# Performance work log

Hardware: AMD Instinct MI355X
Metric: run time of the kernel (lower is better)

The kernel has to match this reference:

```python
import jax, jax.numpy as jnp
import numpy as np

TEMPERATURE = 8.0  # sqrt(d_k=64)

def setup_inputs() -> dict:
    key = jax.random.key(0)
    kq, kk, kv = jax.random.split(key, 3)
    B, S, D = 32, 2048, 64  # B = batch*heads
    q = jax.random.normal(kq, (B, S, D), dtype=jnp.float32)
    k = jax.random.normal(kk, (B, S, D), dtype=jnp.float32)
    v = jax.random.normal(kv, (B, S, D), dtype=jnp.float32)
    return {"q": q, "k": k, "v": v}

def reference(q, k, v):
    # attn = softmax((q @ k^T) / temperature) along key dim; dropout = identity (eval)
    attn = jnp.einsum('bqd,bkd->bqk', q, k) / TEMPERATURE  # [B, S, S]
    attn = jax.nn.softmax(attn, axis=2)
    out = jnp.einsum('bqk,bkd->bqd', attn, v)              # [B, S, D]
    return out
```

## Files before the change

kernel.cpp:

```cpp
#include <hip/hip_runtime.h>
#include <stdint.h>


#define BATCH 32
#define SEQ   2048
#define DIM   64
#define QBLK_WAVE 32
#define NWAVES 4
#define QBLK  (QBLK_WAVE*NWAVES)
#define KVBLK 64
#define NT    (SEQ/KVBLK)
#define BUFSHORTS (KVBLK*DIM)

typedef __attribute__((ext_vector_type(8)))  __bf16   bf16x8;
typedef __attribute__((ext_vector_type(16))) float    f32x16;
typedef __attribute__((ext_vector_type(2)))  unsigned uint2v;
typedef __attribute__((ext_vector_type(4)))  unsigned uint4v;

static __device__ __forceinline__ unsigned cvt_pk(float lo, float hi) {
    unsigned r; asm("v_cvt_pk_bf16_f32 %0, %1, %2" : "=v"(r) : "v"(lo), "v"(hi)); return r;
}
static __device__ __forceinline__ float exp2v(float x) {
    float r; asm("v_exp_f32 %0, %1" : "=v"(r) : "v"(x)); return r;
}
static __device__ __forceinline__ float other_half(float v, int hi) {
    unsigned u = __builtin_bit_cast(unsigned, v);
    uint2v r = __builtin_amdgcn_permlane32_swap(u, u, false, false);
    return __builtin_bit_cast(float, hi ? r[0] : r[1]);
}

#define MFMA32(A, B, C) __builtin_amdgcn_mfma_f32_32x32x16_bf16((A), (B), (C), 0, 0, 0)
#define TRR(dst, OFFSTR) \
    asm volatile("ds_read_b64_tr_b16 %0, %1 offset:" OFFSTR : "=v"(dst) : "v"(trb))
#define MAX4(a,b,c,d) fmaxf(fmaxf((a),(b)), fmaxf((c),(d)))
#define SUM4(a,b,c,d) (((a)+(b)) + ((c)+(d)))

static __device__ __forceinline__ bf16x8 frag_of(uint2v r0, uint2v r1) {
    uint4v w = { r0[0], r0[1], r1[0], r1[1] };
    return __builtin_bit_cast(bf16x8, w);
}

__global__ __launch_bounds__(256, 2)
void attn_fwd_kernel(const float* __restrict__ q,
                     const float* __restrict__ k,
                     const float* __restrict__ v,
                     float* __restrict__ out)
{
    __shared__ unsigned short Ksh[2][BUFSHORTS];
    __shared__ unsigned short Vsh[2][BUFSHORTS];

    const int id    = blockIdx.x;
    const int swz   = (id & 7) * ((SEQ / QBLK) * BATCH / 8) + (id >> 3);
    const int batch = swz >> 4;
    const int qtile = swz & 15;

    const int t    = threadIdx.x;
    const int lane = t & 63;
    const int wid  = t >> 6;
    const int hi   = lane >> 5;
    const int l31  = lane & 31;
    const int l7   = lane & 7;

    const size_t bbase = (size_t)batch * SEQ * DIM;
    const int q0w = qtile * QBLK + wid * QBLK_WAVE;

    bf16x8 qf[4];
    {
        const float sc = 0.125f * 1.44269504088896341f;
        const float* qp = q + bbase + (size_t)(q0w + l31) * DIM + hi * 8;
        #pragma unroll
        for (int dblk = 0; dblk < 4; ++dblk) {
            float4 f0 = *(const float4*)(qp + dblk * 16);
            float4 f1 = *(const float4*)(qp + dblk * 16 + 4);
            uint4v w = { cvt_pk(f0.x * sc, f0.y * sc), cvt_pk(f0.z * sc, f0.w * sc),
                         cvt_pk(f1.x * sc, f1.y * sc), cvt_pk(f1.z * sc, f1.w * sc) };
            qf[dblk] = __builtin_bit_cast(bf16x8, w);
        }
    }

    const int srow = t >> 2, sq = t & 3;
    const float* kg = k + bbase + (size_t)srow * DIM + sq * 16;
    const float* vg = v + bbase + (size_t)srow * DIM + sq * 16;
    const int ch0 = ((2 * sq)     ^ (srow & 7)) * 8;
    const int ch1 = ((2 * sq + 1) ^ (srow & 7)) * 8;

    const int bq = (l31 & 15) >> 2, ee = (lane >> 4) & 1, cc = lane & 3;
    const unsigned vb = (unsigned)(uintptr_t)&Vsh[0][0];
    const unsigned trbase = vb + (unsigned)((8 * hi + bq) * 128 +
                                            (((2 * ee + (cc >> 1)) ^ bq) * 16) + (cc & 1) * 8);

    f32x16 oacc0, oacc1;
    #pragma unroll
    for (int r = 0; r < 16; ++r) { oacc0[r] = 0.f; oacc1[r] = 0.f; }
    float m_run = 0.0f, l_run = 0.0f;

    float4 rk[4], rv[4];
    #pragma unroll
    for (int i = 0; i < 4; ++i) {
        rk[i] = *(const float4*)(kg + i * 4);
        rv[i] = *(const float4*)(vg + i * 4);
    }
    {
        uint4v kw0 = { cvt_pk(rk[0].x, rk[0].y), cvt_pk(rk[0].z, rk[0].w),
                       cvt_pk(rk[1].x, rk[1].y), cvt_pk(rk[1].z, rk[1].w) };
        uint4v kw1 = { cvt_pk(rk[2].x, rk[2].y), cvt_pk(rk[2].z, rk[2].w),
                       cvt_pk(rk[3].x, rk[3].y), cvt_pk(rk[3].z, rk[3].w) };
        uint4v vw0 = { cvt_pk(rv[0].x, rv[0].y), cvt_pk(rv[0].z, rv[0].w),
                       cvt_pk(rv[1].x, rv[1].y), cvt_pk(rv[1].z, rv[1].w) };
        uint4v vw1 = { cvt_pk(rv[2].x, rv[2].y), cvt_pk(rv[2].z, rv[2].w),
                       cvt_pk(rv[3].x, rv[3].y), cvt_pk(rv[3].z, rv[3].w) };
        *(uint4v*)&Ksh[0][srow * DIM + ch0] = kw0;
        *(uint4v*)&Ksh[0][srow * DIM + ch1] = kw1;
        *(uint4v*)&Vsh[0][srow * DIM + ch0] = vw0;
        *(uint4v*)&Vsh[0][srow * DIM + ch1] = vw1;
    }
    #pragma unroll
    for (int i = 0; i < 4; ++i) {
        rk[i] = *(const float4*)(kg + KVBLK * DIM + i * 4);
        rv[i] = *(const float4*)(vg + KVBLK * DIM + i * 4);
    }
    asm volatile("s_waitcnt lgkmcnt(0)" ::: "memory");

    #pragma unroll 2
    for (int tile = 0; tile < NT; ++tile) {
        const int cur = tile & 1;
        __builtin_amdgcn_s_barrier();
        __builtin_amdgcn_sched_barrier(0);

        const unsigned short* krow = &Ksh[cur][l31 * DIM];
        const unsigned trb = trbase + (unsigned)(cur * (2 * BUFSHORTS));

        f32x16 s0, s1;
        #pragma unroll
        for (int r = 0; r < 16; ++r) { s0[r] = 0.f; s1[r] = 0.f; }
        __builtin_amdgcn_s_setprio(1);
        #pragma unroll
        for (int dblk = 0; dblk < 4; ++dblk) {
            int cofs = (((2 * dblk + hi) ^ l7) * 8);
            bf16x8 kf0 = *(const bf16x8*)&krow[cofs];
            bf16x8 kf1 = *(const bf16x8*)&krow[32 * DIM + cofs];
            s0 = MFMA32(kf0, qf[dblk], s0);
            s1 = MFMA32(kf1, qf[dblk], s1);
        }
        __builtin_amdgcn_s_setprio(0);

        uint2v m0k0r0, m0k0r1, m0k1r0, m0k1r1, m0k2r0, m0k2r1, m0k3r0, m0k3r1;
        uint2v m1k0r0, m1k0r1, m1k1r0, m1k1r1, m1k2r0, m1k2r1, m1k3r0, m1k3r1;
        TRR(m0k0r0, "0");    TRR(m0k0r1, "576");
        TRR(m0k1r0, "2048"); TRR(m0k1r1, "2624");
        TRR(m0k2r0, "4096"); TRR(m0k2r1, "4672");
        TRR(m0k3r0, "6144"); TRR(m0k3r1, "6720");
        TRR(m1k0r0, "64");   TRR(m1k0r1, "512");
        TRR(m1k1r0, "2112"); TRR(m1k1r1, "2560");
        TRR(m1k2r0, "4160"); TRR(m1k2r1, "4608");
        TRR(m1k3r0, "6208"); TRR(m1k3r1, "6656");

        {
            float a0 = MAX4(s0[0], s0[1], s0[2],  s0[3]);
            float a1 = MAX4(s0[4], s0[5], s0[6],  s0[7]);
            float a2 = MAX4(s0[8], s0[9], s0[10], s0[11]);
            float a3 = MAX4(s0[12], s0[13], s0[14], s0[15]);
            float b0 = MAX4(s1[0], s1[1], s1[2],  s1[3]);
            float b1 = MAX4(s1[4], s1[5], s1[6],  s1[7]);
            float b2 = MAX4(s1[8], s1[9], s1[10], s1[11]);
            float b3 = MAX4(s1[12], s1[13], s1[14], s1[15]);
            float pmax = MAX4(MAX4(a0, a1, a2, a3), b0, b1, b2);
            pmax = fmaxf(pmax, b3);
            pmax = fmaxf(pmax, other_half(pmax, hi));
            if (!__all(pmax - m_run <= 12.0f)) {
                float mn    = fmaxf(m_run, pmax);
                float alpha = exp2v(m_run - mn);
                m_run = mn;
                l_run *= alpha;
                #pragma unroll
                for (int r = 0; r < 16; ++r) { oacc0[r] *= alpha; oacc1[r] *= alpha; }
            }
        }
        #pragma unroll
        for (int r = 0; r < 16; ++r) s0[r] = exp2v(s0[r] - m_run);
        #pragma unroll
        for (int r = 0; r < 16; ++r) s1[r] = exp2v(s1[r] - m_run);
        {
            float a0 = SUM4(s0[0], s0[1], s0[2],  s0[3]);
            float a1 = SUM4(s0[4], s0[5], s0[6],  s0[7]);
            float a2 = SUM4(s0[8], s0[9], s0[10], s0[11]);
            float a3 = SUM4(s0[12], s0[13], s0[14], s0[15]);
            float b0 = SUM4(s1[0], s1[1], s1[2],  s1[3]);
            float b1 = SUM4(s1[4], s1[5], s1[6],  s1[7]);
            float b2 = SUM4(s1[8], s1[9], s1[10], s1[11]);
            float b3 = SUM4(s1[12], s1[13], s1[14], s1[15]);
            float rs = SUM4(SUM4(a0, a1, a2, a3), b0, b1, b2) + b3;
            rs += other_half(rs, hi);
            l_run += rs;
        }

        bf16x8 bfr0, bfr1, bfr2, bfr3;
        {
            uint2v x1 = __builtin_amdgcn_permlane32_swap(cvt_pk(s0[0], s0[1]),  cvt_pk(s0[4], s0[5]),  false, false);
            uint2v x2 = __builtin_amdgcn_permlane32_swap(cvt_pk(s0[2], s0[3]),  cvt_pk(s0[6], s0[7]),  false, false);
            uint4v w1 = { x1[0], x2[0], x1[1], x2[1] };
            bfr0 = __builtin_bit_cast(bf16x8, w1);
            uint2v y1 = __builtin_amdgcn_permlane32_swap(cvt_pk(s0[8], s0[9]),  cvt_pk(s0[12], s0[13]), false, false);
            uint2v y2 = __builtin_amdgcn_permlane32_swap(cvt_pk(s0[10], s0[11]), cvt_pk(s0[14], s0[15]), false, false);
            uint4v w2 = { y1[0], y2[0], y1[1], y2[1] };
            bfr1 = __builtin_bit_cast(bf16x8, w2);
            uint2v z1 = __builtin_amdgcn_permlane32_swap(cvt_pk(s1[0], s1[1]),  cvt_pk(s1[4], s1[5]),  false, false);
            uint2v z2 = __builtin_amdgcn_permlane32_swap(cvt_pk(s1[2], s1[3]),  cvt_pk(s1[6], s1[7]),  false, false);
            uint4v w3 = { z1[0], z2[0], z1[1], z2[1] };
            bfr2 = __builtin_bit_cast(bf16x8, w3);
            uint2v u1 = __builtin_amdgcn_permlane32_swap(cvt_pk(s1[8], s1[9]),  cvt_pk(s1[12], s1[13]), false, false);
            uint2v u2 = __builtin_amdgcn_permlane32_swap(cvt_pk(s1[10], s1[11]), cvt_pk(s1[14], s1[15]), false, false);
            uint4v w4 = { u1[0], u2[0], u1[1], u2[1] };
            bfr3 = __builtin_bit_cast(bf16x8, w4);
        }

        if (tile + 1 < NT) {
            unsigned short* kst = &Ksh[cur ^ 1][srow * DIM];
            unsigned short* vst = &Vsh[cur ^ 1][srow * DIM];
            uint4v kw0 = { cvt_pk(rk[0].x, rk[0].y), cvt_pk(rk[0].z, rk[0].w),
                           cvt_pk(rk[1].x, rk[1].y), cvt_pk(rk[1].z, rk[1].w) };
            uint4v kw1 = { cvt_pk(rk[2].x, rk[2].y), cvt_pk(rk[2].z, rk[2].w),
                           cvt_pk(rk[3].x, rk[3].y), cvt_pk(rk[3].z, rk[3].w) };
            uint4v vw0 = { cvt_pk(rv[0].x, rv[0].y), cvt_pk(rv[0].z, rv[0].w),
                           cvt_pk(rv[1].x, rv[1].y), cvt_pk(rv[1].z, rv[1].w) };
            uint4v vw1 = { cvt_pk(rv[2].x, rv[2].y), cvt_pk(rv[2].z, rv[2].w),
                           cvt_pk(rv[3].x, rv[3].y), cvt_pk(rv[3].z, rv[3].w) };
            *(uint4v*)&kst[ch0] = kw0;
            *(uint4v*)&kst[ch1] = kw1;
            *(uint4v*)&vst[ch0] = vw0;
            *(uint4v*)&vst[ch1] = vw1;
        }
        if (tile + 2 < NT) {
            const float* kp = kg + (size_t)(tile + 2) * KVBLK * DIM;
            const float* vp = vg + (size_t)(tile + 2) * KVBLK * DIM;
            #pragma unroll
            for (int i = 0; i < 4; ++i) {
                rk[i] = *(const float4*)(kp + i * 4);
                rv[i] = *(const float4*)(vp + i * 4);
            }
        }

        asm volatile("s_waitcnt lgkmcnt(0)" ::: "memory");
        __builtin_amdgcn_sched_barrier(0);

        __builtin_amdgcn_s_setprio(1);
        oacc0 = MFMA32(frag_of(m0k0r0, m0k0r1), bfr0, oacc0);
        oacc1 = MFMA32(frag_of(m1k0r0, m1k0r1), bfr0, oacc1);
        oacc0 = MFMA32(frag_of(m0k1r0, m0k1r1), bfr1, oacc0);
        oacc1 = MFMA32(frag_of(m1k1r0, m1k1r1), bfr1, oacc1);
        oacc0 = MFMA32(frag_of(m0k2r0, m0k2r1), bfr2, oacc0);
        oacc1 = MFMA32(frag_of(m1k2r0, m1k2r1), bfr2, oacc1);
        oacc0 = MFMA32(frag_of(m0k3r0, m0k3r1), bfr3, oacc0);
        oacc1 = MFMA32(frag_of(m1k3r0, m1k3r1), bfr3, oacc1);
        __builtin_amdgcn_s_setprio(0);
    }

    float invl = 1.0f / l_run;
    float* op = out + bbase + (size_t)(q0w + l31) * DIM + 4 * hi;
    #pragma unroll
    for (int rq = 0; rq < 4; ++rq) {
        float4 o0 = { oacc0[4 * rq] * invl, oacc0[4 * rq + 1] * invl,
                      oacc0[4 * rq + 2] * invl, oacc0[4 * rq + 3] * invl };
        float4 o1 = { oacc1[4 * rq] * invl, oacc1[4 * rq + 1] * invl,
                      oacc1[4 * rq + 2] * invl, oacc1[4 * rq + 3] * invl };
        *(float4*)(op + 8 * rq)      = o0;
        *(float4*)(op + 32 + 8 * rq) = o1;
    }
}

extern "C" void kernel_launch(void* const* d_in, const int* in_sizes, int n_in,
                              void* d_out, int out_size, void* d_ws, size_t ws_size,
                              hipStream_t stream) {
    const float* q = (const float*)d_in[0];
    const float* k = (const float*)d_in[1];
    const float* v = (const float*)d_in[2];
    float* out = (float*)d_out;
    dim3 grid((SEQ / QBLK) * BATCH);
    dim3 block(256);
    hipLaunchKernelGGL(attn_fwd_kernel, grid, block, 0, stream, q, k, v, out);
}
```

Baseline: 133.2 us.

## Double KV tile to 128 rows and interleave transposed V reads with PV MFMAs

Raises the KV tile from 64 to 128 rows, so each block does half as many barrier and online-softmax rescale iterations. The next tile's LDS store moves to right after the QK MFMAs. The transposed V reads are now issued in groups and overlapped with the PV MFMAs using partial lgkmcnt waits instead of a single full wait. The trade-off is doubled LDS (64 KB per block, which may cut occupancy below 2 blocks per CU) and more registers for the prefetched K/V and the four score accumulators.

```diff
diff --git a/kernel.cpp b/kernel.cpp
--- a/kernel.cpp
+++ b/kernel.cpp
@@ -8,7 +8,7 @@
 #define QBLK_WAVE 32
 #define NWAVES 4
 #define QBLK  (QBLK_WAVE*NWAVES)
-#define KVBLK 64
+#define KVBLK 128
 #define NT    (SEQ/KVBLK)
 #define BUFSHORTS (KVBLK*DIM)
 
@@ -32,6 +32,14 @@
 #define MFMA32(A, B, C) __builtin_amdgcn_mfma_f32_32x32x16_bf16((A), (B), (C), 0, 0, 0)
 #define TRR(dst, OFFSTR) \
     asm volatile("ds_read_b64_tr_b16 %0, %1 offset:" OFFSTR : "=v"(dst) : "v"(trb))
+#define TRG(KS, A, B, C, D) \
+    do { TRR(ga[KS], A); TRR(gb[KS], B); TRR(gc[KS], C); TRR(gd[KS], D); } while (0)
+#define WAITL(NSTR) \
+    do { asm volatile("s_waitcnt lgkmcnt(" NSTR ")" ::: "memory"); \
+         __builtin_amdgcn_sched_barrier(0); } while (0)
+#define PVK(KS) \
+    do { oacc0 = MFMA32(frag_of(ga[KS], gb[KS]), bfr[KS], oacc0); \
+         oacc1 = MFMA32(frag_of(gc[KS], gd[KS]), bfr[KS], oacc1); } while (0)
 #define MAX4(a,b,c,d) fmaxf(fmaxf((a),(b)), fmaxf((c),(d)))
 #define SUM4(a,b,c,d) (((a)+(b)) + ((c)+(d)))
 
@@ -78,11 +86,13 @@
         }
     }
 
-    const int srow = t >> 2, sq = t & 3;
-    const float* kg = k + bbase + (size_t)srow * DIM + sq * 16;
-    const float* vg = v + bbase + (size_t)srow * DIM + sq * 16;
-    const int ch0 = ((2 * sq)     ^ (srow & 7)) * 8;
-    const int ch1 = ((2 * sq + 1) ^ (srow & 7)) * 8;
+    const int srow = t >> 1, dh = t & 1;
+    const float* kg = k + bbase + (size_t)srow * DIM + dh * 32;
+    const float* vg = v + bbase + (size_t)srow * DIM + dh * 32;
+    const int ch0s = ((4 * dh + 0) ^ (srow & 7)) * 8;
+    const int ch1s = ((4 * dh + 1) ^ (srow & 7)) * 8;
+    const int ch2s = ((4 * dh + 2) ^ (srow & 7)) * 8;
+    const int ch3s = ((4 * dh + 3) ^ (srow & 7)) * 8;
 
     const int bq = (l31 & 15) >> 2, ee = (lane >> 4) & 1, cc = lane & 3;
     const unsigned vb = (unsigned)(uintptr_t)&Vsh[0][0];
@@ -94,28 +104,28 @@
     for (int r = 0; r < 16; ++r) { oacc0[r] = 0.f; oacc1[r] = 0.f; }
     float m_run = 0.0f, l_run = 0.0f;
 
-    float4 rk[4], rv[4];
-    #pragma unroll
-    for (int i = 0; i < 4; ++i) {
+    float4 rk[8], rv[8];
+    #pragma unroll
+    for (int i = 0; i < 8; ++i) {
         rk[i] = *(const float4*)(kg + i * 4);
         rv[i] = *(const float4*)(vg + i * 4);
     }
     {
-        uint4v kw0 = { cvt_pk(rk[0].x, rk[0].y), cvt_pk(rk[0].z, rk[0].w),
-                       cvt_pk(rk[1].x, rk[1].y), cvt_pk(rk[1].z, rk[1].w) };
-        uint4v kw1 = { cvt_pk(rk[2].x, rk[2].y), cvt_pk(rk[2].z, rk[2].w),
-                       cvt_pk(rk[3].x, rk[3].y), cvt_pk(rk[3].z, rk[3].w) };
-        uint4v vw0 = { cvt_pk(rv[0].x, rv[0].y), cvt_pk(rv[0].z, rv[0].w),
-                       cvt_pk(rv[1].x, rv[1].y), cvt_pk(rv[1].z, rv[1].w) };
-        uint4v vw1 = { cvt_pk(rv[2].x, rv[2].y), cvt_pk(rv[2].z, rv[2].w),
-                       cvt_pk(rv[3].x, rv[3].y), cvt_pk(rv[3].z, rv[3].w) };
-        *(uint4v*)&Ksh[0][srow * DIM + ch0] = kw0;
-        *(uint4v*)&Ksh[0][srow * DIM + ch1] = kw1;
-        *(uint4v*)&Vsh[0][srow * DIM + ch0] = vw0;
-        *(uint4v*)&Vsh[0][srow * DIM + ch1] = vw1;
-    }
-    #pragma unroll
-    for (int i = 0; i < 4; ++i) {
+        unsigned short* kst = &Ksh[0][srow * DIM];
+        unsigned short* vst = &Vsh[0][srow * DIM];
+        const int chs[4] = { ch0s, ch1s, ch2s, ch3s };
+        #pragma unroll
+        for (int i2 = 0; i2 < 4; ++i2) {
+            uint4v kw = { cvt_pk(rk[2*i2].x, rk[2*i2].y), cvt_pk(rk[2*i2].z, rk[2*i2].w),
+                          cvt_pk(rk[2*i2+1].x, rk[2*i2+1].y), cvt_pk(rk[2*i2+1].z, rk[2*i2+1].w) };
+            uint4v vw = { cvt_pk(rv[2*i2].x, rv[2*i2].y), cvt_pk(rv[2*i2].z, rv[2*i2].w),
+                          cvt_pk(rv[2*i2+1].x, rv[2*i2+1].y), cvt_pk(rv[2*i2+1].z, rv[2*i2+1].w) };
+            *(uint4v*)&kst[chs[i2]] = kw;
+            *(uint4v*)&vst[chs[i2]] = vw;
+        }
+    }
+    #pragma unroll
+    for (int i = 0; i < 8; ++i) {
         rk[i] = *(const float4*)(kg + KVBLK * DIM + i * 4);
         rv[i] = *(const float4*)(vg + KVBLK * DIM + i * 4);
     }
@@ -130,42 +140,53 @@
         const unsigned short* krow = &Ksh[cur][l31 * DIM];
         const unsigned trb = trbase + (unsigned)(cur * (2 * BUFSHORTS));
 
-        f32x16 s0, s1;
-        #pragma unroll
-        for (int r = 0; r < 16; ++r) { s0[r] = 0.f; s1[r] = 0.f; }
+        f32x16 s[4];
+        #pragma unroll
+        for (int kb = 0; kb < 4; ++kb)
+            #pragma unroll
+            for (int r = 0; r < 16; ++r) s[kb][r] = 0.f;
         __builtin_amdgcn_s_setprio(1);
         #pragma unroll
         for (int dblk = 0; dblk < 4; ++dblk) {
             int cofs = (((2 * dblk + hi) ^ l7) * 8);
-            bf16x8 kf0 = *(const bf16x8*)&krow[cofs];
-            bf16x8 kf1 = *(const bf16x8*)&krow[32 * DIM + cofs];
-            s0 = MFMA32(kf0, qf[dblk], s0);
-            s1 = MFMA32(kf1, qf[dblk], s1);
+            #pragma unroll
+            for (int kb = 0; kb < 4; ++kb) {
+                bf16x8 kf = *(const bf16x8*)&krow[kb * 32 * DIM + cofs];
+                s[kb] = MFMA32(kf, qf[dblk], s[kb]);
+            }
         }
         __builtin_amdgcn_s_setprio(0);
 
-        uint2v m0k0r0, m0k0r1, m0k1r0, m0k1r1, m0k2r0, m0k2r1, m0k3r0, m0k3r1;
-        uint2v m1k0r0, m1k0r1, m1k1r0, m1k1r1, m1k2r0, m1k2r1, m1k3r0, m1k3r1;
-        TRR(m0k0r0, "0");    TRR(m0k0r1, "576");
-        TRR(m0k1r0, "2048"); TRR(m0k1r1, "2624");
-        TRR(m0k2r0, "4096"); TRR(m0k2r1, "4672");
-        TRR(m0k3r0, "6144"); TRR(m0k3r1, "6720");
-        TRR(m1k0r0, "64");   TRR(m1k0r1, "512");
-        TRR(m1k1r0, "2112"); TRR(m1k1r1, "2560");
-        TRR(m1k2r0, "4160"); TRR(m1k2r1, "4608");
-        TRR(m1k3r0, "6208"); TRR(m1k3r1, "6656");
+        if (tile + 1 < NT) {
+            unsigned short* kst = &Ksh[cur ^ 1][srow * DIM];
+            unsigned short* vst = &Vsh[cur ^ 1][srow * DIM];
+            const int chs[4] = { ch0s, ch1s, ch2s, ch3s };
+            #pragma unroll
+            for (int i2 = 0; i2 < 4; ++i2) {
+                uint4v kw = { cvt_pk(rk[2*i2].x, rk[2*i2].y), cvt_pk(rk[2*i2].z, rk[2*i2].w),
+                              cvt_pk(rk[2*i2+1].x, rk[2*i2+1].y), cvt_pk(rk[2*i2+1].z, rk[2*i2+1].w) };
+                uint4v vw = { cvt_pk(rv[2*i2].x, rv[2*i2].y), cvt_pk(rv[2*i2].z, rv[2*i2].w),
+                              cvt_pk(rv[2*i2+1].x, rv[2*i2+1].y), cvt_pk(rv[2*i2+1].z, rv[2*i2+1].w) };
+                *(uint4v*)&kst[chs[i2]] = kw;
+                *(uint4v*)&vst[chs[i2]] = vw;
+            }
+        }
+        __builtin_amdgcn_sched_barrier(0);
+
+        uint2v ga[8], gb[8], gc[8], gd[8];
+        TRG(0, "0",    "576",  "64",   "512");
+        TRG(1, "2048", "2624", "2112", "2560");
 
         {
-            float a0 = MAX4(s0[0], s0[1], s0[2],  s0[3]);
-            float a1 = MAX4(s0[4], s0[5], s0[6],  s0[7]);
-            float a2 = MAX4(s0[8], s0[9], s0[10], s0[11]);
-            float a3 = MAX4(s0[12], s0[13], s0[14], s0[15]);
-            float b0 = MAX4(s1[0], s1[1], s1[2],  s1[3]);
-            float b1 = MAX4(s1[4], s1[5], s1[6],  s1[7]);
-            float b2 = MAX4(s1[8], s1[9], s1[10], s1[11]);
-            float b3 = MAX4(s1[12], s1[13], s1[14], s1[15]);
-            float pmax = MAX4(MAX4(a0, a1, a2, a3), b0, b1, b2);
-            pmax = fmaxf(pmax, b3);
+            float mx[16];
+            #pragma unroll
+            for (int r = 0; r < 16; ++r)
+                mx[r] = MAX4(s[0][r], s[1][r], s[2][r], s[3][r]);
+            float p0 = MAX4(mx[0],  mx[1],  mx[2],  mx[3]);
+            float p1 = MAX4(mx[4],  mx[5],  mx[6],  mx[7]);
+            float p2 = MAX4(mx[8],  mx[9],  mx[10], mx[11]);
+            float p3 = MAX4(mx[12], mx[13], mx[14], mx[15]);
+            float pmax = MAX4(p0, p1, p2, p3);
             pmax = fmaxf(pmax, other_half(pmax, hi));
             if (!__all(pmax - m_run <= 12.0f)) {
                 float mn    = fmaxf(m_run, pmax);
@@ -177,82 +198,61 @@
             }
         }
         #pragma unroll
-        for (int r = 0; r < 16; ++r) s0[r] = exp2v(s0[r] - m_run);
-        #pragma unroll
-        for (int r = 0; r < 16; ++r) s1[r] = exp2v(s1[r] - m_run);
+        for (int kb = 0; kb < 4; ++kb)
+            #pragma unroll
+            for (int r = 0; r < 16; ++r) s[kb][r] = exp2v(s[kb][r] - m_run);
         {
-            float a0 = SUM4(s0[0], s0[1], s0[2],  s0[3]);
-            float a1 = SUM4(s0[4], s0[5], s0[6],  s0[7]);
-            float a2 = SUM4(s0[8], s0[9], s0[10], s0[11]);
-            float a3 = SUM4(s0[12], s0[13], s0[14], s0[15]);
-            float b0 = SUM4(s1[0], s1[1], s1[2],  s1[3]);
-            float b1 = SUM4(s1[4], s1[5], s1[6],  s1[7]);
-            float b2 = SUM4(s1[8], s1[9], s1[10], s1[11]);
-            float b3 = SUM4(s1[12], s1[13], s1[14], s1[15]);
-            float rs = SUM4(SUM4(a0, a1, a2, a3), b0, b1, b2) + b3;
+            float sx[16];
+            #pragma unroll
+            for (int r = 0; r < 16; ++r)
+                sx[r] = SUM4(s[0][r], s[1][r], s[2][r], s[3][r]);
+            float q0s = SUM4(sx[0],  sx[1],  sx[2],  sx[3]);
+            float q1s = SUM4(sx[4],  sx[5],  sx[6],  sx[7]);
+            float q2s = SUM4(sx[8],  sx[9],  sx[10], sx[11]);
+            float q3s = SUM4(sx[12], sx[13], sx[14], sx[15]);
+            float rs = SUM4(q0s, q1s, q2s, q3s);
             rs += other_half(rs, hi);
             l_run += rs;
         }
 
-        bf16x8 bfr0, bfr1, bfr2, bfr3;
-        {
-            uint2v x1 = __builtin_amdgcn_permlane32_swap(cvt_pk(s0[0], s0[1]),  cvt_pk(s0[4], s0[5]),  false, false);
-            uint2v x2 = __builtin_amdgcn_permlane32_swap(cvt_pk(s0[2], s0[3]),  cvt_pk(s0[6], s0[7]),  false, false);
+        bf16x8 bfr[8];
+        #pragma unroll
+        for (int kb = 0; kb < 4; ++kb) {
+            uint2v x1 = __builtin_amdgcn_permlane32_swap(cvt_pk(s[kb][0],  s[kb][1]),
+                                                         cvt_pk(s[kb][4],  s[kb][5]),  false, false);
+            uint2v x2 = __builtin_amdgcn_permlane32_swap(cvt_pk(s[kb][2],  s[kb][3]),
+                                                         cvt_pk(s[kb][6],  s[kb][7]),  false, false);
             uint4v w1 = { x1[0], x2[0], x1[1], x2[1] };
-            bfr0 = __builtin_bit_cast(bf16x8, w1);
-            uint2v y1 = __builtin_amdgcn_permlane32_swap(cvt_pk(s0[8], s0[9]),  cvt_pk(s0[12], s0[13]), false, false);
-            uint2v y2 = __builtin_amdgcn_permlane32_swap(cvt_pk(s0[10], s0[11]), cvt_pk(s0[14], s0[15]), false, false);
+            bfr[2*kb] = __builtin_bit_cast(bf16x8, w1);
+            uint2v y1 = __builtin_amdgcn_permlane32_swap(cvt_pk(s[kb][8],  s[kb][9]),
+                                                         cvt_pk(s[kb][12], s[kb][13]), false, false);
+            uint2v y2 = __builtin_amdgcn_permlane32_swap(cvt_pk(s[kb][10], s[kb][11]),
+                                                         cvt_pk(s[kb][14], s[kb][15]), false, false);
             uint4v w2 = { y1[0], y2[0], y1[1], y2[1] };
-            bfr1 = __builtin_bit_cast(bf16x8, w2);
-            uint2v z1 = __builtin_amdgcn_permlane32_swap(cvt_pk(s1[0], s1[1]),  cvt_pk(s1[4], s1[5]),  false, false);
-            uint2v z2 = __builtin_amdgcn_permlane32_swap(cvt_pk(s1[2], s1[3]),  cvt_pk(s1[6], s1[7]),  false, false);
-            uint4v w3 = { z1[0], z2[0], z1[1], z2[1] };
-            bfr2 = __builtin_bit_cast(bf16x8, w3);
-            uint2v u1 = __builtin_amdgcn_permlane32_swap(cvt_pk(s1[8], s1[9]),  cvt_pk(s1[12], s1[13]), false, false);
-            uint2v u2 = __builtin_amdgcn_permlane32_swap(cvt_pk(s1[10], s1[11]), cvt_pk(s1[14], s1[15]), false, false);
-            uint4v w4 = { u1[0], u2[0], u1[1], u2[1] };
-            bfr3 = __builtin_bit_cast(bf16x8, w4);
-        }
-
-        if (tile + 1 < NT) {
-            unsigned short* kst = &Ksh[cur ^ 1][srow * DIM];
-            unsigned short* vst = &Vsh[cur ^ 1][srow * DIM];
-            uint4v kw0 = { cvt_pk(rk[0].x, rk[0].y), cvt_pk(rk[0].z, rk[0].w),
-                           cvt_pk(rk[1].x, rk[1].y), cvt_pk(rk[1].z, rk[1].w) };
-            uint4v kw1 = { cvt_pk(rk[2].x, rk[2].y), cvt_pk(rk[2].z, rk[2].w),
-                           cvt_pk(rk[3].x, rk[3].y), cvt_pk(rk[3].z, rk[3].w) };
-            uint4v vw0 = { cvt_pk(rv[0].x, rv[0].y), cvt_pk(rv[0].z, rv[0].w),
-                           cvt_pk(rv[1].x, rv[1].y), cvt_pk(rv[1].z, rv[1].w) };
-            uint4v vw1 = { cvt_pk(rv[2].x, rv[2].y), cvt_pk(rv[2].z, rv[2].w),
-                           cvt_pk(rv[3].x, rv[3].y), cvt_pk(rv[3].z, rv[3].w) };
-            *(uint4v*)&kst[ch0] = kw0;
-            *(uint4v*)&kst[ch1] = kw1;
-            *(uint4v*)&vst[ch0] = vw0;
-            *(uint4v*)&vst[ch1] = vw1;
-        }
+            bfr[2*kb+1] = __builtin_bit_cast(bf16x8, w2);
+        }
+
+        __builtin_amdgcn_s_setprio(1);
+        TRG(2, "4096",  "4672",  "4160",  "4608");
+        WAITL("8");  PVK(0);  TRG(3, "6144",  "6720",  "6208",  "6656");
+        WAITL("8");  PVK(1);  TRG(4, "8192",  "8768",  "8256",  "8704");
+        WAITL("8");  PVK(2);  TRG(5, "10240", "10816", "10304", "10752");
+        WAITL("8");  PVK(3);  TRG(6, "12288", "12864", "12352", "12800");
+        WAITL("8");  PVK(4);  TRG(7, "14336", "14912", "14400", "14848");
+        WAITL("8");  PVK(5);
+        WAITL("4");  PVK(6);
+        WAITL("0");  PVK(7);
+        __builtin_amdgcn_s_setprio(0);
+
         if (tile + 2 < NT) {
             const float* kp = kg + (size_t)(tile + 2) * KVBLK * DIM;
             const float* vp = vg + (size_t)(tile + 2) * KVBLK * DIM;
             #pragma unroll
-            for (int i = 0; i < 4; ++i) {
+            for (int i = 0; i < 8; ++i) {
                 rk[i] = *(const float4*)(kp + i * 4);
                 rv[i] = *(const float4*)(vp + i * 4);
             }
         }
-
-        asm volatile("s_waitcnt lgkmcnt(0)" ::: "memory");
-        __builtin_amdgcn_sched_barrier(0);
-
-        __builtin_amdgcn_s_setprio(1);
-        oacc0 = MFMA32(frag_of(m0k0r0, m0k0r1), bfr0, oacc0);
-        oacc1 = MFMA32(frag_of(m1k0r0, m1k0r1), bfr0, oacc1);
-        oacc0 = MFMA32(frag_of(m0k1r0, m0k1r1), bfr1, oacc0);
-        oacc1 = MFMA32(frag_of(m1k1r0, m1k1r1), bfr1, oacc1);
-        oacc0 = MFMA32(frag_of(m0k2r0, m0k2r1), bfr2, oacc0);
-        oacc1 = MFMA32(frag_of(m1k2r0, m1k2r1), bfr2, oacc1);
-        oacc0 = MFMA32(frag_of(m0k3r0, m0k3r1), bfr3, oacc0);
-        oacc1 = MFMA32(frag_of(m1k3r0, m1k3r1), bfr3, oacc1);
-        __builtin_amdgcn_s_setprio(0);
     }
 
     float invl = 1.0f / l_run;
```

Result: slower. 152.9 us (+14.8%).

## Reorder LDS staging and prefetch, use max3 reduction and fast exp path

Applied to the files above, without the earlier changes.

Moves the bf16 conversion and LDS store of the next K/V tile to right after the QK MFMAs, and moves the global prefetch of tile+2 to after the PV MFMAs. The aim is to overlap LDS writes with the softmax math and to shorten register lifetimes. It also replaces the pairwise max tree with v_max3, swaps the inline-asm bf16 pack for compiler casts, and adds a branch that skips the subtraction when the running max is still zero. Register pressure and scheduling may shift, and the extra wave-uniform branch adds a little control overhead.

```diff
diff --git a/kernel.cpp b/kernel.cpp
--- a/kernel.cpp
+++ b/kernel.cpp
@@ -13,15 +13,21 @@
 #define BUFSHORTS (KVBLK*DIM)
 
 typedef __attribute__((ext_vector_type(8)))  __bf16   bf16x8;
+typedef __attribute__((ext_vector_type(2)))  __bf16   bf16x2;
 typedef __attribute__((ext_vector_type(16))) float    f32x16;
 typedef __attribute__((ext_vector_type(2)))  unsigned uint2v;
 typedef __attribute__((ext_vector_type(4)))  unsigned uint4v;
 
-static __device__ __forceinline__ unsigned cvt_pk(float lo, float hi) {
-    unsigned r; asm("v_cvt_pk_bf16_f32 %0, %1, %2" : "=v"(r) : "v"(lo), "v"(hi)); return r;
+static __device__ __forceinline__ unsigned pk(float lo, float hi) {
+    bf16x2 p; p[0] = (__bf16)lo; p[1] = (__bf16)hi;
+    return __builtin_bit_cast(unsigned, p);
 }
 static __device__ __forceinline__ float exp2v(float x) {
     float r; asm("v_exp_f32 %0, %1" : "=v"(r) : "v"(x)); return r;
+}
+static __device__ __forceinline__ float max3(float a, float b, float c) {
+    float d; asm("v_max3_f32 %0, %1, %2, %3" : "=v"(d) : "v"(a), "v"(b), "v"(c));
+    return d;
 }
 static __device__ __forceinline__ float other_half(float v, int hi) {
     unsigned u = __builtin_bit_cast(unsigned, v);
@@ -32,7 +38,6 @@
 #define MFMA32(A, B, C) __builtin_amdgcn_mfma_f32_32x32x16_bf16((A), (B), (C), 0, 0, 0)
 #define TRR(dst, OFFSTR) \
     asm volatile("ds_read_b64_tr_b16 %0, %1 offset:" OFFSTR : "=v"(dst) : "v"(trb))
-#define MAX4(a,b,c,d) fmaxf(fmaxf((a),(b)), fmaxf((c),(d)))
 #define SUM4(a,b,c,d) (((a)+(b)) + ((c)+(d)))
 
 static __device__ __forceinline__ bf16x8 frag_of(uint2v r0, uint2v r1) {
@@ -72,11 +77,12 @@
         for (int dblk = 0; dblk < 4; ++dblk) {
             float4 f0 = *(const float4*)(qp + dblk * 16);
             float4 f1 = *(const float4*)(qp + dblk * 16 + 4);
-            uint4v w = { cvt_pk(f0.x * sc, f0.y * sc), cvt_pk(f0.z * sc, f0.w * sc),
-                         cvt_pk(f1.x * sc, f1.y * sc), cvt_pk(f1.z * sc, f1.w * sc) };
+            uint4v w = { pk(f0.x * sc, f0.y * sc), pk(f0.z * sc, f0.w * sc),
+                         pk(f1.x * sc, f1.y * sc), pk(f1.z * sc, f1.w * sc) };
             qf[dblk] = __builtin_bit_cast(bf16x8, w);
         }
     }
+    asm("" : "+v"(qf[0]), "+v"(qf[1]), "+v"(qf[2]), "+v"(qf[3]));
 
     const int srow = t >> 2, sq = t & 3;
     const float* kg = k + bbase + (size_t)srow * DIM + sq * 16;
@@ -101,14 +107,14 @@
         rv[i] = *(const float4*)(vg + i * 4);
     }
     {
-        uint4v kw0 = { cvt_pk(rk[0].x, rk[0].y), cvt_pk(rk[0].z, rk[0].w),
-                       cvt_pk(rk[1].x, rk[1].y), cvt_pk(rk[1].z, rk[1].w) };
-        uint4v kw1 = { cvt_pk(rk[2].x, rk[2].y), cvt_pk(rk[2].z, rk[2].w),
-                       cvt_pk(rk[3].x, rk[3].y), cvt_pk(rk[3].z, rk[3].w) };
-        uint4v vw0 = { cvt_pk(rv[0].x, rv[0].y), cvt_pk(rv[0].z, rv[0].w),
-                       cvt_pk(rv[1].x, rv[1].y), cvt_pk(rv[1].z, rv[1].w) };
-        uint4v vw1 = { cvt_pk(rv[2].x, rv[2].y), cvt_pk(rv[2].z, rv[2].w),
-                       cvt_pk(rv[3].x, rv[3].y), cvt_pk(rv[3].z, rv[3].w) };
+        uint4v kw0 = { pk(rk[0].x, rk[0].y), pk(rk[0].z, rk[0].w),
+                       pk(rk[1].x, rk[1].y), pk(rk[1].z, rk[1].w) };
+        uint4v kw1 = { pk(rk[2].x, rk[2].y), pk(rk[2].z, rk[2].w),
+                       pk(rk[3].x, rk[3].y), pk(rk[3].z, rk[3].w) };
+        uint4v vw0 = { pk(rv[0].x, rv[0].y), pk(rv[0].z, rv[0].w),
+                       pk(rv[1].x, rv[1].y), pk(rv[1].z, rv[1].w) };
+        uint4v vw1 = { pk(rv[2].x, rv[2].y), pk(rv[2].z, rv[2].w),
+                       pk(rv[3].x, rv[3].y), pk(rv[3].z, rv[3].w) };
         *(uint4v*)&Ksh[0][srow * DIM + ch0] = kw0;
         *(uint4v*)&Ksh[0][srow * DIM + ch1] = kw1;
         *(uint4v*)&Vsh[0][srow * DIM + ch0] = vw0;
@@ -143,6 +149,24 @@
             s1 = MFMA32(kf1, qf[dblk], s1);
         }
         __builtin_amdgcn_s_setprio(0);
+        asm("" : "+v"(s0), "+v"(s1));
+
+        if (tile + 1 < NT) {
+            unsigned short* kst = &Ksh[cur ^ 1][srow * DIM];
+            unsigned short* vst = &Vsh[cur ^ 1][srow * DIM];
+            uint4v kw0 = { pk(rk[0].x, rk[0].y), pk(rk[0].z, rk[0].w),
+                           pk(rk[1].x, rk[1].y), pk(rk[1].z, rk[1].w) };
+            uint4v kw1 = { pk(rk[2].x, rk[2].y), pk(rk[2].z, rk[2].w),
+                           pk(rk[3].x, rk[3].y), pk(rk[3].z, rk[3].w) };
+            uint4v vw0 = { pk(rv[0].x, rv[0].y), pk(rv[0].z, rv[0].w),
+                           pk(rv[1].x, rv[1].y), pk(rv[1].z, rv[1].w) };
+            uint4v vw1 = { pk(rv[2].x, rv[2].y), pk(rv[2].z, rv[2].w),
+                           pk(rv[3].x, rv[3].y), pk(rv[3].z, rv[3].w) };
+            *(uint4v*)&kst[ch0] = kw0;
+            *(uint4v*)&kst[ch1] = kw1;
+            *(uint4v*)&vst[ch0] = vw0;
+            *(uint4v*)&vst[ch1] = vw1;
+        }
 
         uint2v m0k0r0, m0k0r1, m0k1r0, m0k1r1, m0k2r0, m0k2r1, m0k3r0, m0k3r1;
         uint2v m1k0r0, m1k0r1, m1k1r0, m1k1r1, m1k2r0, m1k2r1, m1k3r0, m1k3r1;
@@ -156,16 +180,22 @@
         TRR(m1k3r0, "6208"); TRR(m1k3r1, "6656");
 
         {
-            float a0 = MAX4(s0[0], s0[1], s0[2],  s0[3]);
-            float a1 = MAX4(s0[4], s0[5], s0[6],  s0[7]);
-            float a2 = MAX4(s0[8], s0[9], s0[10], s0[11]);
-            float a3 = MAX4(s0[12], s0[13], s0[14], s0[15]);
-            float b0 = MAX4(s1[0], s1[1], s1[2],  s1[3]);
-            float b1 = MAX4(s1[4], s1[5], s1[6],  s1[7]);
-            float b2 = MAX4(s1[8], s1[9], s1[10], s1[11]);
-            float b3 = MAX4(s1[12], s1[13], s1[14], s1[15]);
-            float pmax = MAX4(MAX4(a0, a1, a2, a3), b0, b1, b2);
-            pmax = fmaxf(pmax, b3);
+            float t0 = max3(s0[0],  s0[1],  s0[2]);
+            float t1 = max3(s0[3],  s0[4],  s0[5]);
+            float t2 = max3(s0[6],  s0[7],  s0[8]);
+            float t3 = max3(s0[9],  s0[10], s0[11]);
+            float t4 = max3(s0[12], s0[13], s0[14]);
+            float t5 = max3(s0[15], s1[0],  s1[1]);
+            float t6 = max3(s1[2],  s1[3],  s1[4]);
+            float t7 = max3(s1[5],  s1[6],  s1[7]);
+            float t8 = max3(s1[8],  s1[9],  s1[10]);
+            float t9 = max3(s1[11], s1[12], s1[13]);
+            float ta = fmaxf(s1[14], s1[15]);
+            float u0 = max3(t0, t1, t2);
+            float u1 = max3(t3, t4, t5);
+            float u2 = max3(t6, t7, t8);
+            float u3 = max3(t9, ta, u0);
+            float pmax = max3(u1, u2, u3);
             pmax = fmaxf(pmax, other_half(pmax, hi));
             if (!__all(pmax - m_run <= 12.0f)) {
                 float mn    = fmaxf(m_run, pmax);
@@ -176,10 +206,17 @@
                 for (int r = 0; r < 16; ++r) { oacc0[r] *= alpha; oacc1[r] *= alpha; }
             }
         }
-        #pragma unroll
-        for (int r = 0; r < 16; ++r) s0[r] = exp2v(s0[r] - m_run);
-        #pragma unroll
-        for (int r = 0; r < 16; ++r) s1[r] = exp2v(s1[r] - m_run);
+        if (__all(m_run == 0.0f)) {
+            #pragma unroll
+            for (int r = 0; r < 16; ++r) s0[r] = exp2v(s0[r]);
+            #pragma unroll
+            for (int r = 0; r < 16; ++r) s1[r] = exp2v(s1[r]);
+        } else {
+            #pragma unroll
+            for (int r = 0; r < 16; ++r) s0[r] = exp2v(s0[r] - m_run);
+            #pragma unroll
+            for (int r = 0; r < 16; ++r) s1[r] = exp2v(s1[r] - m_run);
+        }
         {
             float a0 = SUM4(s0[0], s0[1], s0[2],  s0[3]);
             float a1 = SUM4(s0[4], s0[5], s0[6],  s0[7]);
@@ -196,48 +233,22 @@
 
         bf16x8 bfr0, bfr1, bfr2, bfr3;
         {
-            uint2v x1 = __builtin_amdgcn_permlane32_swap(cvt_pk(s0[0], s0[1]),  cvt_pk(s0[4], s0[5]),  false, false);
-            uint2v x2 = __builtin_amdgcn_permlane32_swap(cvt_pk(s0[2], s0[3]),  cvt_pk(s0[6], s0[7]),  false, false);
+            uint2v x1 = __builtin_amdgcn_permlane32_swap(pk(s0[0], s0[1]),  pk(s0[4], s0[5]),  false, false);
+            uint2v x2 = __builtin_amdgcn_permlane32_swap(pk(s0[2], s0[3]),  pk(s0[6], s0[7]),  false, false);
             uint4v w1 = { x1[0], x2[0], x1[1], x2[1] };
             bfr0 = __builtin_bit_cast(bf16x8, w1);
-            uint2v y1 = __builtin_amdgcn_permlane32_swap(cvt_pk(s0[8], s0[9]),  cvt_pk(s0[12], s0[13]), false, false);
-            uint2v y2 = __builtin_amdgcn_permlane32_swap(cvt_pk(s0[10], s0[11]), cvt_pk(s0[14], s0[15]), false, false);
+            uint2v y1 = __builtin_amdgcn_permlane32_swap(pk(s0[8], s0[9]),  pk(s0[12], s0[13]), false, false);
+            uint2v y2 = __builtin_amdgcn_permlane32_swap(pk(s0[10], s0[11]), pk(s0[14], s0[15]), false, false);
             uint4v w2 = { y1[0], y2[0], y1[1], y2[1] };
             bfr1 = __builtin_bit_cast(bf16x8, w2);
-            uint2v z1 = __builtin_amdgcn_permlane32_swap(cvt_pk(s1[0], s1[1]),  cvt_pk(s1[4], s1[5]),  false, false);
-            uint2v z2 = __builtin_amdgcn_permlane32_swap(cvt_pk(s1[2], s1[3]),  cvt_pk(s1[6], s1[7]),  false, false);
+            uint2v z1 = __builtin_amdgcn_permlane32_swap(pk(s1[0], s1[1]),  pk(s1[4], s1[5]),  false, false);
+            uint2v z2 = __builtin_amdgcn_permlane32_swap(pk(s1[2], s1[3]),  pk(s1[6], s1[7]),  false, false);
             uint4v w3 = { z1[0], z2[0], z1[1], z2[1] };
             bfr2 = __builtin_bit_cast(bf16x8, w3);
-            uint2v u1 = __builtin_amdgcn_permlane32_swap(cvt_pk(s1[8], s1[9]),  cvt_pk(s1[12], s1[13]), false, false);
-            uint2v u2 = __builtin_amdgcn_permlane32_swap(cvt_pk(s1[10], s1[11]), cvt_pk(s1[14], s1[15]), false, false);
+            uint2v u1 = __builtin_amdgcn_permlane32_swap(pk(s1[8], s1[9]),  pk(s1[12], s1[13]), false, false);
+            uint2v u2 = __builtin_amdgcn_permlane32_swap(pk(s1[10], s1[11]), pk(s1[14], s1[15]), false, false);
             uint4v w4 = { u1[0], u2[0], u1[1], u2[1] };
             bfr3 = __builtin_bit_cast(bf16x8, w4);
-        }
-
-        if (tile + 1 < NT) {
-            unsigned short* kst = &Ksh[cur ^ 1][srow * DIM];
-            unsigned short* vst = &Vsh[cur ^ 1][srow * DIM];
-            uint4v kw0 = { cvt_pk(rk[0].x, rk[0].y), cvt_pk(rk[0].z, rk[0].w),
-                           cvt_pk(rk[1].x, rk[1].y), cvt_pk(rk[1].z, rk[1].w) };
-            uint4v kw1 = { cvt_pk(rk[2].x, rk[2].y), cvt_pk(rk[2].z, rk[2].w),
-                           cvt_pk(rk[3].x, rk[3].y), cvt_pk(rk[3].z, rk[3].w) };
-            uint4v vw0 = { cvt_pk(rv[0].x, rv[0].y), cvt_pk(rv[0].z, rv[0].w),
-                           cvt_pk(rv[1].x, rv[1].y), cvt_pk(rv[1].z, rv[1].w) };
-            uint4v vw1 = { cvt_pk(rv[2].x, rv[2].y), cvt_pk(rv[2].z, rv[2].w),
-                           cvt_pk(rv[3].x, rv[3].y), cvt_pk(rv[3].z, rv[3].w) };
-            *(uint4v*)&kst[ch0] = kw0;
-            *(uint4v*)&kst[ch1] = kw1;
-            *(uint4v*)&vst[ch0] = vw0;
-            *(uint4v*)&vst[ch1] = vw1;
-        }
-        if (tile + 2 < NT) {
-            const float* kp = kg + (size_t)(tile + 2) * KVBLK * DIM;
-            const float* vp = vg + (size_t)(tile + 2) * KVBLK * DIM;
-            #pragma unroll
-            for (int i = 0; i < 4; ++i) {
-                rk[i] = *(const float4*)(kp + i * 4);
-                rv[i] = *(const float4*)(vp + i * 4);
-            }
         }
 
         asm volatile("s_waitcnt lgkmcnt(0)" ::: "memory");
@@ -253,6 +264,16 @@
         oacc0 = MFMA32(frag_of(m0k3r0, m0k3r1), bfr3, oacc0);
         oacc1 = MFMA32(frag_of(m1k3r0, m1k3r1), bfr3, oacc1);
         __builtin_amdgcn_s_setprio(0);
+
+        if (tile + 2 < NT) {
+            const float* kp = kg + (size_t)(tile + 2) * KVBLK * DIM;
+            const float* vp = vg + (size_t)(tile + 2) * KVBLK * DIM;
+            #pragma unroll
+            for (int i = 0; i < 4; ++i) {
+                rk[i] = *(const float4*)(kp + i * 4);
+                rv[i] = *(const float4*)(vp + i * 4);
+            }
+        }
     }
 
     float invl = 1.0f / l_run;
```

Measured after the change: 131.2 us. Within noise of the previous version (-1.5%).
